# Optimization experiments

Measured on AMD Instinct MI355X. Metric: run time of the kernel, lower is better.

The kernel has to match this reference:

```python
import jax, jax.numpy as jnp
import numpy as np

H_DIM = 1024
MAX_T = 1024
N_HEADS = 16


def setup_inputs() -> dict:
    key = jax.random.key(0)
    ks = jax.random.split(key, 9)
    B, T, C = 4, 1024, H_DIM
    s = 1.0 / np.sqrt(C)
    return {
        "x": jax.random.normal(ks[0], (B, T, C), jnp.float32),
        "Wq": jax.random.normal(ks[1], (C, H_DIM), jnp.float32) * s,
        "bq": jnp.zeros((H_DIM,), jnp.float32),
        "Wk": jax.random.normal(ks[2], (C, H_DIM), jnp.float32) * s,
        "bk": jnp.zeros((H_DIM,), jnp.float32),
        "Wv": jax.random.normal(ks[3], (C, H_DIM), jnp.float32) * s,
        "bv": jnp.zeros((H_DIM,), jnp.float32),
        "Wo": jax.random.normal(ks[4], (H_DIM, H_DIM), jnp.float32) * s,
        "bo": jnp.zeros((H_DIM,), jnp.float32),
    }


def reference(x, Wq, bq, Wk, bk, Wv, bv, Wo, bo):
    B, T, C = x.shape
    N, D = N_HEADS, C // N_HEADS
    # QKV projections -> [B, N, T, D]
    def split_heads(y):
        return y.reshape(B, T, N, D).transpose(0, 2, 1, 3)
    q = split_heads(x @ Wq + bq)
    k = split_heads(x @ Wk + bk)
    v = split_heads(x @ Wv + bv)
    # scores [B, N, T, T]
    scores = jnp.einsum("bntd,bnsd->bnts", q, k) / jnp.sqrt(jnp.float32(D))
    # Faithful to source: -1e9 added on the LOWER-triangular positions
    mask = jnp.tril(jnp.ones((T, T), jnp.float32)) * (-1e9)
    scores = scores + mask[None, None, :, :]
    attn = jax.nn.softmax(scores, axis=-1)
    out = jnp.einsum("bnts,bnsd->bntd", attn, v)  # [B, N, T, D]
    out = out.transpose(0, 2, 1, 3).reshape(B, T, N * D)
    return out @ Wo + bo
```

## Files before the change

kernel.cpp:

```cpp
#include <hip/hip_runtime.h>
#include <hip/hip_bf16.h>
#include <stdint.h>

#define T_SEQ 1024
#define C_DIM 1024
#define NH 16
#define DH 64

typedef __attribute__((ext_vector_type(8))) __bf16 bf16x8;
typedef __attribute__((ext_vector_type(8))) uint16_t u16x8;
typedef __attribute__((ext_vector_type(4))) float f32x4;

__device__ __forceinline__ uint16_t f2bf(float f) {
    union { float f; uint32_t u; } v; v.f = f;
    uint32_t u = v.u;
    return (uint16_t)((u + 0x7FFFu + ((u >> 16) & 1u)) >> 16);
}
__device__ __forceinline__ float bf2f(uint16_t b) {
    union { uint32_t u; float f; } v; v.u = ((uint32_t)b) << 16; return v.f;
}

__global__ void k_prep(const float* __restrict__ x,
                       const float* __restrict__ W0, const float* __restrict__ W1,
                       const float* __restrict__ W2, const float* __restrict__ W3,
                       uint16_t* __restrict__ xb, uint16_t* __restrict__ wout) {
    const int gid = blockIdx.x;
    if (gid < 2048) {
        int i = gid * 256 + threadIdx.x;
        const int st = 2048 * 256;
#pragma unroll
        for (int it = 0; it < 2; it++, i += st) {
            float4 v = reinterpret_cast<const float4*>(x)[i];
            ushort4 o;
            o.x = f2bf(v.x); o.y = f2bf(v.y); o.z = f2bf(v.z); o.w = f2bf(v.w);
            reinterpret_cast<ushort4*>(xb)[i] = o;
        }
        return;
    }
    __shared__ float tile[32][33];
    const int id2 = gid - 2048;
    const int z = id2 >> 10;
    const int by = ((id2 >> 5) & 31) * 32;
    const int bx = (id2 & 31) * 32;
    const float* in = (z == 0) ? W0 : (z == 1) ? W1 : (z == 2) ? W2 : W3;
    uint16_t* o = wout + ((size_t)z << 20);
    const int tx = threadIdx.x & 31, ty = threadIdx.x >> 5;
#pragma unroll
    for (int i = 0; i < 4; i++)
        tile[ty + i * 8][tx] = in[(size_t)(by + ty + i * 8) * C_DIM + bx + tx];
    __syncthreads();
#pragma unroll
    for (int i = 0; i < 4; i++)
        o[(size_t)(bx + ty + i * 8) * C_DIM + by + tx] = f2bf(tile[tx][ty + i * 8]);
}

__global__ void k_vmean(const uint16_t* __restrict__ Vt, float* __restrict__ Vmean) {
    const int bh = blockIdx.x;
    const int tid = threadIdx.x;
    const int d = tid >> 2, part = tid & 3;
    const uint16_t* src = Vt + ((size_t)bh * DH + d) * T_SEQ + part * 256;
    float s = 0.f;
#pragma unroll
    for (int i = 0; i < 32; i++) {
        u16x8 v = *reinterpret_cast<const u16x8*>(src + i * 8);
#pragma unroll
        for (int j = 0; j < 8; j++) s += bf2f(v[j]);
    }
    s += __shfl_xor(s, 1);
    s += __shfl_xor(s, 2);
    if (part == 0) Vmean[bh * DH + d] = s * (1.0f / 1024.0f);
}

__device__ __forceinline__ void stage_g(const uint16_t* A, const uint16_t* Bt, int bm, int bn,
                                        int kt, char* la, char* lb, int tid) {
    const int w = tid >> 6, srow = tid >> 2;
    const int scol = (((tid & 3) ^ ((srow >> 1) & 3))) * 8;
#pragma unroll
    for (int p = 0; p < 2; p++) {
        const uint16_t* ga = A + (size_t)(bm + p * 64 + srow) * C_DIM + kt + scol;
        const uint16_t* gb = Bt + (size_t)(bn + p * 64 + srow) * C_DIM + kt + scol;
        __builtin_amdgcn_global_load_lds(
            (const __attribute__((address_space(1))) void*)ga,
            (__attribute__((address_space(3))) void*)(la + p * 4096 + w * 1024), 16, 0, 0);
        __builtin_amdgcn_global_load_lds(
            (const __attribute__((address_space(1))) void*)gb,
            (__attribute__((address_space(3))) void*)(lb + p * 4096 + w * 1024), 16, 0, 0);
    }
}

__global__ __launch_bounds__(256) void k_gemm_qkv(const uint16_t* __restrict__ A,
                                                  const uint16_t* __restrict__ Bt,
                                                  const float* __restrict__ bq,
                                                  const float* __restrict__ bk,
                                                  const float* __restrict__ bv,
                                                  uint16_t* __restrict__ qb,
                                                  uint16_t* __restrict__ kb,
                                                  uint16_t* __restrict__ vt) {
    __shared__ uint16_t lA[128 * 32];
    __shared__ uint16_t lB[128 * 32];
    const int bm = blockIdx.x * 128;
    const int bn = blockIdx.y * 128;
    const int tid = threadIdx.x;
    const int lane = tid & 63;
    const int w = tid >> 6;
    const int wm = (w >> 1) * 64;
    const int wn = (w & 1) * 64;
    const int ko = (lane >> 4) * 8;
    const int rr = lane & 15;
    const int pos = ko ^ (((rr >> 1) & 3) << 3);

    f32x4 acc[4][4] = {};

    for (int kt = 0; kt < C_DIM; kt += 32) {
        stage_g(A, Bt, bm, bn, kt, (char*)lA, (char*)lB, tid);
        __syncthreads();
        bf16x8 af[4], bfr[4];
#pragma unroll
        for (int i = 0; i < 4; i++) {
            af[i]  = *reinterpret_cast<const bf16x8*>(&lA[(wm + i * 16 + rr) * 32 + pos]);
            bfr[i] = *reinterpret_cast<const bf16x8*>(&lB[(wn + i * 16 + rr) * 32 + pos]);
        }
#pragma unroll
        for (int mi = 0; mi < 4; mi++)
#pragma unroll
            for (int ni = 0; ni < 4; ni++)
                acc[mi][ni] = __builtin_amdgcn_mfma_f32_16x16x32_bf16(af[mi], bfr[ni], acc[mi][ni], 0, 0, 0);
        __syncthreads();
    }

    const float* bias; uint16_t* outp; int coff, vmode;
    if (bn < 1024)      { bias = bq; outp = qb; coff = 0;    vmode = 0; }
    else if (bn < 2048) { bias = bk; outp = kb; coff = 1024; vmode = 0; }
    else                { bias = bv; outp = vt; coff = 2048; vmode = 1; }

    const int r0 = (lane >> 4) * 4;
    const int cc = lane & 15;
#pragma unroll
    for (int ni = 0; ni < 4; ni++) {
        const int colg = bn + wn + ni * 16 + cc;
        const int col = colg - coff;
        const float bvv = bias[col];
#pragma unroll
        for (int mi = 0; mi < 4; mi++) {
#pragma unroll
            for (int jj = 0; jj < 4; jj++) {
                const int row = bm + wm + mi * 16 + r0 + jj;
                float v = acc[mi][ni][jj] + bvv;
                if (vmode == 0) {
                    outp[(size_t)row * C_DIM + col] = f2bf(v);
                } else {
                    const int b = row >> 10, t2 = row & 1023;
                    const int h = col >> 6, d = col & 63;
                    outp[((size_t)((b * NH + h) * DH + d) << 10) + t2] = f2bf(v);
                }
            }
        }
    }
}

__global__ __launch_bounds__(256) void k_gemm_o(const uint16_t* __restrict__ A,
                                                const uint16_t* __restrict__ Bt,
                                                const float* __restrict__ bias,
                                                float* __restrict__ Out) {
    __shared__ uint16_t lA[128 * 32];
    __shared__ uint16_t lB[128 * 32];
    const int bm = blockIdx.x * 128;
    const int bn = blockIdx.y * 128;
    const int tid = threadIdx.x;
    const int lane = tid & 63;
    const int w = tid >> 6;
    const int wm = (w >> 1) * 64;
    const int wn = (w & 1) * 64;
    const int ko = (lane >> 4) * 8;
    const int rr = lane & 15;
    const int pos = ko ^ (((rr >> 1) & 3) << 3);

    f32x4 acc[4][4] = {};

    for (int kt = 0; kt < C_DIM; kt += 32) {
        stage_g(A, Bt, bm, bn, kt, (char*)lA, (char*)lB, tid);
        __syncthreads();
        bf16x8 af[4], bfr[4];
#pragma unroll
        for (int i = 0; i < 4; i++) {
            af[i]  = *reinterpret_cast<const bf16x8*>(&lA[(wm + i * 16 + rr) * 32 + pos]);
            bfr[i] = *reinterpret_cast<const bf16x8*>(&lB[(wn + i * 16 + rr) * 32 + pos]);
        }
#pragma unroll
        for (int mi = 0; mi < 4; mi++)
#pragma unroll
            for (int ni = 0; ni < 4; ni++)
                acc[mi][ni] = __builtin_amdgcn_mfma_f32_16x16x32_bf16(af[mi], bfr[ni], acc[mi][ni], 0, 0, 0);
        __syncthreads();
    }

    const int r0 = (lane >> 4) * 4;
    const int cc = lane & 15;
#pragma unroll
    for (int ni = 0; ni < 4; ni++) {
        const int col = bn + wn + ni * 16 + cc;
        const float bvv = bias[col];
#pragma unroll
        for (int mi = 0; mi < 4; mi++)
#pragma unroll
            for (int jj = 0; jj < 4; jj++) {
                const int row = bm + wm + mi * 16 + r0 + jj;
                Out[(size_t)row * C_DIM + col] = acc[mi][ni][jj] + bvv;
            }
    }
}

__global__ __launch_bounds__(256, 3) void k_attn(const uint16_t* __restrict__ Q,
                                                 const uint16_t* __restrict__ Kb,
                                                 const uint16_t* __restrict__ Vt,
                                                 const float* __restrict__ Vmean,
                                                 uint16_t* __restrict__ Ob) {
    __shared__ char smem[32768 + 4 * 4608];
    const int tid = threadIdx.x;
    const int lane = tid & 63;
    const int w = tid >> 6;
    uint16_t* lpLo = reinterpret_cast<uint16_t*>(smem + 32768 + w * 4608);
    uint16_t* lpHi = lpLo + 1152;

    const int id = blockIdx.x;
    const int bh = id & 63;
    const int braw = id >> 6;
    const int b = (braw < 4) ? braw : 11 - braw;
    const int q0 = b * 128;
    const int bb = bh >> 4, h = bh & 15;
    const int qq = lane & 15;
    const int gg = lane >> 4;
    const int ko = gg * 8;
    const int r0 = gg * 4;
    const int qgLo = q0 + w * 32 + qq;
    const int qgHi = qgLo + 16;

    const uint16_t* qpLo = Q + (size_t)(bb * T_SEQ + qgLo) * C_DIM + h * DH + ko;
    const uint16_t* qpHi = Q + (size_t)(bb * T_SEQ + qgHi) * C_DIM + h * DH + ko;
    bf16x8 bqLo0 = *reinterpret_cast<const bf16x8*>(qpLo);
    bf16x8 bqLo1 = *reinterpret_cast<const bf16x8*>(qpLo + 32);
    bf16x8 bqHi0 = *reinterpret_cast<const bf16x8*>(qpHi);
    bf16x8 bqHi1 = *reinterpret_cast<const bf16x8*>(qpHi + 32);

    const uint16_t* kbase = Kb + (size_t)bb * T_SEQ * C_DIM + h * DH;
    const uint16_t* vbase = Vt + (size_t)bh * DH * T_SEQ;
    const uint16_t* KL = reinterpret_cast<const uint16_t*>(smem);
    const uint16_t* VL = reinterpret_cast<const uint16_t*>(smem + 16384);

    f32x4 oLo[4] = {}, oHi[4] = {};
    float llLo = 0.f, llHi = 0.f;
    const float zs = 0.125f * 1.44269504088896f;

    const int sz = (qq & 7) << 3;

    const int t0 = b;
    for (int t = t0; t < 8; t++) {
        const int s0 = t * 128;
#pragma unroll
        for (int i = 0; i < 4; i++) {
            const int r = i * 32 + (tid >> 3);
            const int sc = ((tid & 7) ^ (r & 7)) * 8;
            const uint16_t* ks = kbase + (size_t)(s0 + r) * C_DIM + sc;
            __builtin_amdgcn_global_load_lds(
                (const __attribute__((address_space(1))) void*)ks,
                (__attribute__((address_space(3))) void*)(smem + i * 4096 + w * 1024), 16, 0, 0);
        }
#pragma unroll
        for (int i = 0; i < 4; i++) {
            const int r = i * 16 + (tid >> 4);
            const int sc = ((tid & 15) ^ (r & 7)) * 8;
            const uint16_t* vs = vbase + (size_t)r * T_SEQ + s0 + sc;
            __builtin_amdgcn_global_load_lds(
                (const __attribute__((address_space(1))) void*)vs,
                (__attribute__((address_space(3))) void*)(smem + 16384 + i * 4096 + w * 1024), 16, 0, 0);
        }
        __syncthreads();

        uint32_t* lpLo32 = reinterpret_cast<uint32_t*>(lpLo);
        uint32_t* lpHi32 = reinterpret_cast<uint32_t*>(lpHi);
#pragma unroll
        for (int h2 = 0; h2 < 2; h2++) {
#pragma unroll
            for (int hf = 0; hf < 4; hf++) {
                const int rr = h2 * 64 + hf * 16 + qq;
                bf16x8 kf0 = *reinterpret_cast<const bf16x8*>(&KL[rr * 64 + (ko ^ sz)]);
                bf16x8 kf1 = *reinterpret_cast<const bf16x8*>(&KL[rr * 64 + ((32 + ko) ^ sz)]);
                f32x4 sLo = {}, sHi = {};
                sLo = __builtin_amdgcn_mfma_f32_16x16x32_bf16(kf0, bqLo0, sLo, 0, 0, 0);
                sLo = __builtin_amdgcn_mfma_f32_16x16x32_bf16(kf1, bqLo1, sLo, 0, 0, 0);
                sHi = __builtin_amdgcn_mfma_f32_16x16x32_bf16(kf0, bqHi0, sHi, 0, 0, 0);
                sHi = __builtin_amdgcn_mfma_f32_16x16x32_bf16(kf1, bqHi1, sHi, 0, 0, 0);
#pragma unroll
                for (int j = 0; j < 4; j++) {
                    const int k = s0 + h2 * 64 + hf * 16 + r0 + j;
                    const float zLo = sLo[j] * zs + ((k <= qgLo) ? -1e9f : 0.0f);
                    const float zHi = sHi[j] * zs + ((k <= qgHi) ? -1e9f : 0.0f);
                    const float pLo = __builtin_amdgcn_exp2f(zLo);
                    const float pHi = __builtin_amdgcn_exp2f(zHi);
                    sLo[j] = pLo; llLo += pLo;
                    sHi[j] = pHi; llHi += pHi;
                }
#pragma unroll
                for (int jp = 0; jp < 2; jp++) {
                    union { __hip_bfloat162 h2u; uint32_t u; } cL, cH;
                    cL.h2u = __float22bfloat162_rn(make_float2(sLo[2 * jp], sLo[2 * jp + 1]));
                    cH.h2u = __float22bfloat162_rn(make_float2(sHi[2 * jp], sHi[2 * jp + 1]));
                    lpLo32[qq * 36 + hf * 8 + (r0 >> 1) + jp] = cL.u;
                    lpHi32[qq * 36 + hf * 8 + (r0 >> 1) + jp] = cH.u;
                }
            }
            bf16x8 paLo0 = *reinterpret_cast<const bf16x8*>(&lpLo[qq * 72 + ko]);
            bf16x8 paLo1 = *reinterpret_cast<const bf16x8*>(&lpLo[qq * 72 + 32 + ko]);
            bf16x8 paHi0 = *reinterpret_cast<const bf16x8*>(&lpHi[qq * 72 + ko]);
            bf16x8 paHi1 = *reinterpret_cast<const bf16x8*>(&lpHi[qq * 72 + 32 + ko]);
#pragma unroll
            for (int ni = 0; ni < 4; ni++) {
                const int rr = ni * 16 + qq;
                bf16x8 vf0 = *reinterpret_cast<const bf16x8*>(&VL[rr * 128 + ((h2 * 64 + ko) ^ sz)]);
                bf16x8 vf1 = *reinterpret_cast<const bf16x8*>(&VL[rr * 128 + ((h2 * 64 + 32 + ko) ^ sz)]);
                oLo[ni] = __builtin_amdgcn_mfma_f32_16x16x32_bf16(paLo0, vf0, oLo[ni], 0, 0, 0);
                oLo[ni] = __builtin_amdgcn_mfma_f32_16x16x32_bf16(paLo1, vf1, oLo[ni], 0, 0, 0);
                oHi[ni] = __builtin_amdgcn_mfma_f32_16x16x32_bf16(paHi0, vf0, oHi[ni], 0, 0, 0);
                oHi[ni] = __builtin_amdgcn_mfma_f32_16x16x32_bf16(paHi1, vf1, oHi[ni], 0, 0, 0);
            }
        }
        __syncthreads();
    }

    llLo += __shfl_xor(llLo, 16); llLo += __shfl_xor(llLo, 32);
    llHi += __shfl_xor(llHi, 16); llHi += __shfl_xor(llHi, 32);
#pragma unroll
    for (int j = 0; j < 4; j++) {
        {
            const float lr = __shfl(llLo, r0 + j);
            const size_t row = (size_t)(bb * T_SEQ + q0 + w * 32 + r0 + j);
            if (lr > 0.f) {
                const float rinv = 1.0f / lr;
#pragma unroll
                for (int ni = 0; ni < 4; ni++)
                    Ob[row * C_DIM + h * DH + ni * 16 + qq] = f2bf(oLo[ni][j] * rinv);
            } else {
#pragma unroll
                for (int ni = 0; ni < 4; ni++)
                    Ob[row * C_DIM + h * DH + ni * 16 + qq] = f2bf(Vmean[bh * DH + ni * 16 + qq]);
            }
        }
        {
            const float lr = __shfl(llHi, r0 + j);
            const size_t row = (size_t)(bb * T_SEQ + q0 + w * 32 + 16 + r0 + j);
            if (lr > 0.f) {
                const float rinv = 1.0f / lr;
#pragma unroll
                for (int ni = 0; ni < 4; ni++)
                    Ob[row * C_DIM + h * DH + ni * 16 + qq] = f2bf(oHi[ni][j] * rinv);
            } else {
#pragma unroll
                for (int ni = 0; ni < 4; ni++)
                    Ob[row * C_DIM + h * DH + ni * 16 + qq] = f2bf(Vmean[bh * DH + ni * 16 + qq]);
            }
        }
    }
}

extern "C" void kernel_launch(void* const* d_in, const int* in_sizes, int n_in,
                              void* d_out, int out_size, void* d_ws, size_t ws_size,
                              hipStream_t stream) {
    const float* x  = (const float*)d_in[0];
    const float* Wq = (const float*)d_in[1];
    const float* bq = (const float*)d_in[2];
    const float* Wk = (const float*)d_in[3];
    const float* bk = (const float*)d_in[4];
    const float* Wv = (const float*)d_in[5];
    const float* bv = (const float*)d_in[6];
    const float* Wo = (const float*)d_in[7];
    const float* bo = (const float*)d_in[8];
    float* out = (float*)d_out;

    char* ws = (char*)d_ws;
    uint16_t* xb    = (uint16_t*)(ws);
    uint16_t* wqkvt = (uint16_t*)(ws + (8u  << 20));
    float*    vmean = (float*)   (ws + (12u << 20));
    uint16_t* qb    = (uint16_t*)(ws + (16u << 20));
    uint16_t* kb    = (uint16_t*)(ws + (24u << 20));
    uint16_t* vt    = (uint16_t*)(ws + (32u << 20));
    uint16_t* wot   = wqkvt + (3u << 20);
    uint16_t* ab    = qb;

    k_prep<<<6144, 256, 0, stream>>>(x, Wq, Wk, Wv, Wo, xb, wqkvt);

    k_gemm_qkv<<<dim3(32, 24), 256, 0, stream>>>(xb, wqkvt, bq, bk, bv, qb, kb, vt);
    k_vmean<<<64, 256, 0, stream>>>(vt, vmean);
    k_attn<<<512, 256, 0, stream>>>(qb, kb, vt, vmean, ab);
    k_gemm_o<<<dim3(32, 8), 256, 0, stream>>>(ab, wot, bo, out);
}
```

Baseline: 103.2 us.

## Double-buffer LDS in QKV and output GEMMs to overlap global loads with MFMA

Replaces the single-buffered K-loop in both projection GEMMs with a two-stage LDS ping-pong. The next K-tile is fetched via global_load_lds while MFMAs run on the current tile, and waiting is done with an explicit vmcnt(4) plus raw s_barrier. This aims to hide global-load latency that previously stalled every iteration. It doubles LDS use per block, which may lower occupancy, and the hand-counted vmcnt depends on stage_g issuing exactly four loads.

```diff
diff --git a/kernel.cpp b/kernel.cpp
--- a/kernel.cpp
+++ b/kernel.cpp
@@ -88,6 +88,37 @@
     }
 }
 
+#define GEMM_KLOOP(LA, LB)                                                        \
+    stage_g(A, Bt, bm, bn, 0, (char*)LA[0], (char*)LB[0], tid);                   \
+    for (int kt = 0; kt < 32; kt++) {                                             \
+        const int c = kt & 1;                                                     \
+        if (kt < 31) {                                                            \
+            stage_g(A, Bt, bm, bn, (kt + 1) * 32, (char*)LA[c ^ 1], (char*)LB[c ^ 1], tid); \
+            __builtin_amdgcn_sched_barrier(0);                                    \
+            asm volatile("s_waitcnt vmcnt(4)" ::: "memory");                      \
+        } else {                                                                  \
+            __builtin_amdgcn_sched_barrier(0);                                    \
+            asm volatile("s_waitcnt vmcnt(0)" ::: "memory");                      \
+        }                                                                         \
+        __builtin_amdgcn_sched_barrier(0);                                        \
+        __builtin_amdgcn_s_barrier();       \
+        __builtin_amdgcn_sched_barrier(0);                                        \
+        bf16x8 af[4], bfr[4];                                                     \
+        _Pragma("unroll")                                                         \
+        for (int i = 0; i < 4; i++) {                                             \
+            af[i]  = *reinterpret_cast<const bf16x8*>(&LA[c][(wm + i * 16 + rr) * 32 + pos]); \
+            bfr[i] = *reinterpret_cast<const bf16x8*>(&LB[c][(wn + i * 16 + rr) * 32 + pos]); \
+        }                                                                         \
+        _Pragma("unroll")                                                         \
+        for (int mi = 0; mi < 4; mi++)                                            \
+            _Pragma("unroll")                                                     \
+            for (int ni = 0; ni < 4; ni++)                                        \
+                acc[mi][ni] = __builtin_amdgcn_mfma_f32_16x16x32_bf16(af[mi], bfr[ni], acc[mi][ni], 0, 0, 0); \
+        __builtin_amdgcn_sched_barrier(0);                                        \
+        __builtin_amdgcn_s_barrier();       \
+        __builtin_amdgcn_sched_barrier(0);                                        \
+    }
+
 __global__ __launch_bounds__(256) void k_gemm_qkv(const uint16_t* __restrict__ A,
                                                   const uint16_t* __restrict__ Bt,
                                                   const float* __restrict__ bq,
@@ -96,8 +127,8 @@
                                                   uint16_t* __restrict__ qb,
                                                   uint16_t* __restrict__ kb,
                                                   uint16_t* __restrict__ vt) {
-    __shared__ uint16_t lA[128 * 32];
-    __shared__ uint16_t lB[128 * 32];
+    __shared__ uint16_t lA[2][128 * 32];
+    __shared__ uint16_t lB[2][128 * 32];
     const int bm = blockIdx.x * 128;
     const int bn = blockIdx.y * 128;
     const int tid = threadIdx.x;
@@ -111,22 +142,7 @@
 
     f32x4 acc[4][4] = {};
 
-    for (int kt = 0; kt < C_DIM; kt += 32) {
-        stage_g(A, Bt, bm, bn, kt, (char*)lA, (char*)lB, tid);
-        __syncthreads();
-        bf16x8 af[4], bfr[4];
-#pragma unroll
-        for (int i = 0; i < 4; i++) {
-            af[i]  = *reinterpret_cast<const bf16x8*>(&lA[(wm + i * 16 + rr) * 32 + pos]);
-            bfr[i] = *reinterpret_cast<const bf16x8*>(&lB[(wn + i * 16 + rr) * 32 + pos]);
-        }
-#pragma unroll
-        for (int mi = 0; mi < 4; mi++)
-#pragma unroll
-            for (int ni = 0; ni < 4; ni++)
-                acc[mi][ni] = __builtin_amdgcn_mfma_f32_16x16x32_bf16(af[mi], bfr[ni], acc[mi][ni], 0, 0, 0);
-        __syncthreads();
-    }
+    GEMM_KLOOP(lA, lB)
 
     const float* bias; uint16_t* outp; int coff, vmode;
     if (bn < 1024)      { bias = bq; outp = qb; coff = 0;    vmode = 0; }
@@ -162,8 +178,8 @@
                                                 const uint16_t* __restrict__ Bt,
                                                 const float* __restrict__ bias,
                                                 float* __restrict__ Out) {
-    __shared__ uint16_t lA[128 * 32];
-    __shared__ uint16_t lB[128 * 32];
+    __shared__ uint16_t lA[2][128 * 32];
+    __shared__ uint16_t lB[2][128 * 32];
     const int bm = blockIdx.x * 128;
     const int bn = blockIdx.y * 128;
     const int tid = threadIdx.x;
@@ -177,22 +193,7 @@
 
     f32x4 acc[4][4] = {};
 
-    for (int kt = 0; kt < C_DIM; kt += 32) {
-        stage_g(A, Bt, bm, bn, kt, (char*)lA, (char*)lB, tid);
-        __syncthreads();
-        bf16x8 af[4], bfr[4];
-#pragma unroll
-        for (int i = 0; i < 4; i++) {
-            af[i]  = *reinterpret_cast<const bf16x8*>(&lA[(wm + i * 16 + rr) * 32 + pos]);
-            bfr[i] = *reinterpret_cast<const bf16x8*>(&lB[(wn + i * 16 + rr) * 32 + pos]);
-        }
-#pragma unroll
-        for (int mi = 0; mi < 4; mi++)
-#pragma unroll
-            for (int ni = 0; ni < 4; ni++)
-                acc[mi][ni] = __builtin_amdgcn_mfma_f32_16x16x32_bf16(af[mi], bfr[ni], acc[mi][ni], 0, 0, 0);
-        __syncthreads();
-    }
+    GEMM_KLOOP(lA, lB)
 
     const int r0 = (lane >> 4) * 4;
     const int cc = lane & 15;
```

New measurement: 106.8 us. 3.6% more time.

## Rewrite QKV GEMM with 256x256 tiles and double-buffered async LDS pipeline

Applied to the files above, without the earlier changes.

Replaces the 128x128, K=32 single-buffered QKV GEMM with a 512-thread kernel computing 256x256 tiles with K=64 steps, double-buffered LDS filled by global_load_lds and staged in quarters interleaved with MFMA phases. It uses explicit vmcnt waits, XOR swizzling, and setprio around MFMA bursts to overlap loads with compute and improve operand reuse. The trade-off is only 192 blocks on the device and large LDS use, which reduces occupancy and may leave compute units idle.

```diff
diff --git a/kernel.cpp b/kernel.cpp
--- a/kernel.cpp
+++ b/kernel.cpp
@@ -69,6 +69,133 @@
     s += __shfl_xor(s, 1);
     s += __shfl_xor(s, 2);
     if (part == 0) Vmean[bh * DH + d] = s * (1.0f / 1024.0f);
+}
+
+__device__ __forceinline__ void stage_half(const uint16_t* __restrict__ src, int rowbase,
+                                           int kt, char* ldsbase, int tid) {
+    const int wid = tid >> 6;
+#pragma unroll
+    for (int i = 0; i < 2; i++) {
+        const int r = i * 64 + (tid >> 3);
+        const int sch = (tid & 7) ^ (r & 7);
+        const uint16_t* g = src + (size_t)(rowbase + r) * C_DIM + kt * 64 + sch * 8;
+        __builtin_amdgcn_global_load_lds(
+            (const __attribute__((address_space(1))) void*)g,
+            (__attribute__((address_space(3))) void*)(ldsbase + i * 8192 + wid * 1024),
+            16, 0, 0);
+    }
+}
+
+__global__ __launch_bounds__(512) void k_gemm_qkv(const uint16_t* __restrict__ A,
+                                                  const uint16_t* __restrict__ Bt,
+                                                  const float* __restrict__ bq,
+                                                  const float* __restrict__ bk,
+                                                  const float* __restrict__ bv,
+                                                  uint16_t* __restrict__ qb,
+                                                  uint16_t* __restrict__ kb,
+                                                  uint16_t* __restrict__ vt) {
+    __shared__ uint16_t lA[2][256 * 64];
+    __shared__ uint16_t lB[2][256 * 64];
+    const int tid = threadIdx.x;
+    const int lane = tid & 63;
+    const int wid = tid >> 6;
+    const int wr = wid >> 2;
+    const int wc = wid & 3;
+    const int bm = blockIdx.x * 256;
+    const int bn = blockIdx.y * 256;
+    const int qq = lane & 15;
+    const int gg = lane >> 4;
+    const int r0 = gg * 4;
+
+    f32x4 acc[8][4] = {};
+
+    stage_half(A,  bm,       0, (char*)lA[0],         tid);
+    stage_half(A,  bm + 128, 0, (char*)lA[0] + 16384, tid);
+    stage_half(Bt, bn,       0, (char*)lB[0],         tid);
+    stage_half(Bt, bn + 128, 0, (char*)lB[0] + 16384, tid);
+
+#pragma unroll 1
+    for (int kt = 0; kt < 16; kt++) {
+        const int c = kt & 1;
+        const uint16_t* LAc = lA[c];
+        const uint16_t* LBc = lB[c];
+        char* LAn = (char*)lA[c ^ 1];
+        char* LBn = (char*)lB[c ^ 1];
+#pragma unroll
+        for (int p = 0; p < 4; p++) {
+            if (kt < 15) {
+                if (p == 0) stage_half(A,  bm,       kt + 1, LAn,         tid);
+                if (p == 1) stage_half(A,  bm + 128, kt + 1, LAn + 16384, tid);
+                if (p == 2) stage_half(Bt, bn,       kt + 1, LBn,         tid);
+                if (p == 3) stage_half(Bt, bn + 128, kt + 1, LBn + 16384, tid);
+            }
+            if (p == 0) {
+                __builtin_amdgcn_sched_barrier(0);
+                if (kt < 15) asm volatile("s_waitcnt vmcnt(2)" ::: "memory");
+                else         asm volatile("s_waitcnt vmcnt(0)" ::: "memory");
+                __builtin_amdgcn_sched_barrier(0);
+            }
+            __builtin_amdgcn_s_barrier();
+            const int mh = p >> 1, nh = p & 1;
+            bf16x8 af[4][2], bfr[2][2];
+#pragma unroll
+            for (int m = 0; m < 4; m++) {
+                const int row = wr * 128 + mh * 64 + m * 16 + qq;
+#pragma unroll
+                for (int kk = 0; kk < 2; kk++) {
+                    const int pos = ((kk * 4 + gg) ^ (qq & 7)) * 8;
+                    af[m][kk] = *reinterpret_cast<const bf16x8*>(&LAc[row * 64 + pos]);
+                }
+            }
+#pragma unroll
+            for (int n = 0; n < 2; n++) {
+                const int row = wc * 64 + nh * 32 + n * 16 + qq;
+#pragma unroll
+                for (int kk = 0; kk < 2; kk++) {
+                    const int pos = ((kk * 4 + gg) ^ (qq & 7)) * 8;
+                    bfr[n][kk] = *reinterpret_cast<const bf16x8*>(&LBc[row * 64 + pos]);
+                }
+            }
+            __builtin_amdgcn_s_setprio(1);
+#pragma unroll
+            for (int m = 0; m < 4; m++)
+#pragma unroll
+                for (int n = 0; n < 2; n++)
+#pragma unroll
+                    for (int kk = 0; kk < 2; kk++)
+                        acc[mh * 4 + m][nh * 2 + n] = __builtin_amdgcn_mfma_f32_16x16x32_bf16(
+                            af[m][kk], bfr[n][kk], acc[mh * 4 + m][nh * 2 + n], 0, 0, 0);
+            __builtin_amdgcn_s_setprio(0);
+            __builtin_amdgcn_s_barrier();
+        }
+    }
+
+    const float* bias; uint16_t* outp; int coff, vmode;
+    if (bn < 1024)      { bias = bq; outp = qb; coff = 0;    vmode = 0; }
+    else if (bn < 2048) { bias = bk; outp = kb; coff = 1024; vmode = 0; }
+    else                { bias = bv; outp = vt; coff = 2048; vmode = 1; }
+
+#pragma unroll
+    for (int n = 0; n < 4; n++) {
+        const int colg = bn + wc * 64 + n * 16 + qq;
+        const int col = colg - coff;
+        const float bvv = bias[col];
+#pragma unroll
+        for (int mi = 0; mi < 8; mi++) {
+#pragma unroll
+            for (int jj = 0; jj < 4; jj++) {
+                const int row = bm + wr * 128 + (mi >> 2) * 64 + (mi & 3) * 16 + r0 + jj;
+                float v = acc[mi][n][jj] + bvv;
+                if (vmode == 0) {
+                    outp[(size_t)row * C_DIM + col] = f2bf(v);
+                } else {
+                    const int b = row >> 10, t2 = row & 1023;
+                    const int h = col >> 6, d = col & 63;
+                    outp[((size_t)((b * NH + h) * DH + d) << 10) + t2] = f2bf(v);
+                }
+            }
+        }
+    }
 }
 
 __device__ __forceinline__ void stage_g(const uint16_t* A, const uint16_t* Bt, int bm, int bn,
@@ -85,76 +212,6 @@
         __builtin_amdgcn_global_load_lds(
             (const __attribute__((address_space(1))) void*)gb,
             (__attribute__((address_space(3))) void*)(lb + p * 4096 + w * 1024), 16, 0, 0);
-    }
-}
-
-__global__ __launch_bounds__(256) void k_gemm_qkv(const uint16_t* __restrict__ A,
-                                                  const uint16_t* __restrict__ Bt,
-                                                  const float* __restrict__ bq,
-                                                  const float* __restrict__ bk,
-                                                  const float* __restrict__ bv,
-                                                  uint16_t* __restrict__ qb,
-                                                  uint16_t* __restrict__ kb,
-                                                  uint16_t* __restrict__ vt) {
-    __shared__ uint16_t lA[128 * 32];
-    __shared__ uint16_t lB[128 * 32];
-    const int bm = blockIdx.x * 128;
-    const int bn = blockIdx.y * 128;
-    const int tid = threadIdx.x;
-    const int lane = tid & 63;
-    const int w = tid >> 6;
-    const int wm = (w >> 1) * 64;
-    const int wn = (w & 1) * 64;
-    const int ko = (lane >> 4) * 8;
-    const int rr = lane & 15;
-    const int pos = ko ^ (((rr >> 1) & 3) << 3);
-
-    f32x4 acc[4][4] = {};
-
-    for (int kt = 0; kt < C_DIM; kt += 32) {
-        stage_g(A, Bt, bm, bn, kt, (char*)lA, (char*)lB, tid);
-        __syncthreads();
-        bf16x8 af[4], bfr[4];
-#pragma unroll
-        for (int i = 0; i < 4; i++) {
-            af[i]  = *reinterpret_cast<const bf16x8*>(&lA[(wm + i * 16 + rr) * 32 + pos]);
-            bfr[i] = *reinterpret_cast<const bf16x8*>(&lB[(wn + i * 16 + rr) * 32 + pos]);
-        }
-#pragma unroll
-        for (int mi = 0; mi < 4; mi++)
-#pragma unroll
-            for (int ni = 0; ni < 4; ni++)
-                acc[mi][ni] = __builtin_amdgcn_mfma_f32_16x16x32_bf16(af[mi], bfr[ni], acc[mi][ni], 0, 0, 0);
-        __syncthreads();
-    }
-
-    const float* bias; uint16_t* outp; int coff, vmode;
-    if (bn < 1024)      { bias = bq; outp = qb; coff = 0;    vmode = 0; }
-    else if (bn < 2048) { bias = bk; outp = kb; coff = 1024; vmode = 0; }
-    else                { bias = bv; outp = vt; coff = 2048; vmode = 1; }
-
-    const int r0 = (lane >> 4) * 4;
-    const int cc = lane & 15;
-#pragma unroll
-    for (int ni = 0; ni < 4; ni++) {
-        const int colg = bn + wn + ni * 16 + cc;
-        const int col = colg - coff;
-        const float bvv = bias[col];
-#pragma unroll
-        for (int mi = 0; mi < 4; mi++) {
-#pragma unroll
-            for (int jj = 0; jj < 4; jj++) {
-                const int row = bm + wm + mi * 16 + r0 + jj;
-                float v = acc[mi][ni][jj] + bvv;
-                if (vmode == 0) {
-                    outp[(size_t)row * C_DIM + col] = f2bf(v);
-                } else {
-                    const int b = row >> 10, t2 = row & 1023;
-                    const int h = col >> 6, d = col & 63;
-                    outp[((size_t)((b * NH + h) * DH + d) << 10) + t2] = f2bf(v);
-                }
-            }
-        }
     }
 }
 
@@ -388,7 +445,7 @@
 
     k_prep<<<6144, 256, 0, stream>>>(x, Wq, Wk, Wv, Wo, xb, wqkvt);
 
-    k_gemm_qkv<<<dim3(32, 24), 256, 0, stream>>>(xb, wqkvt, bq, bk, bv, qb, kb, vt);
+    k_gemm_qkv<<<dim3(16, 12), 512, 0, stream>>>(xb, wqkvt, bq, bk, bv, qb, kb, vt);
     k_vmean<<<64, 256, 0, stream>>>(vt, vmean);
     k_attn<<<512, 256, 0, stream>>>(qb, kb, vt, vmean, ab);
     k_gemm_o<<<dim3(32, 8), 256, 0, stream>>>(ab, wot, bo, out);
```

New measurement: 142.7 us. 1.38x slower.

## Double-buffer K tiles in LDS and load V fragments directly from global

Applied to the files above, without the earlier changes.

The attention kernel now prefetches the next K tile into a second LDS buffer while computing on the current one, and drops the trailing barrier. V fragments are read straight from global memory into registers instead of being staged in LDS. On the first (diagonal) tile, waves whose queries fall entirely in the masked region skip the first half. This overlaps K loading with compute and cuts LDS traffic, at the cost of uncoalesced-ish global V reads and more register pressure.

```diff
diff --git a/kernel.cpp b/kernel.cpp
--- a/kernel.cpp
+++ b/kernel.cpp
@@ -244,8 +244,6 @@
 
     const uint16_t* kbase = Kb + (size_t)bb * T_SEQ * C_DIM + h * DH;
     const uint16_t* vbase = Vt + (size_t)bh * DH * T_SEQ;
-    const uint16_t* KL = reinterpret_cast<const uint16_t*>(smem);
-    const uint16_t* VL = reinterpret_cast<const uint16_t*>(smem + 16384);
 
     f32x4 oLo[4] = {}, oHi[4] = {};
     float llLo = 0.f, llHi = 0.f;
@@ -254,32 +252,46 @@
     const int sz = (qq & 7) << 3;
 
     const int t0 = b;
+#pragma unroll
+    for (int i = 0; i < 4; i++) {
+        const int r = i * 32 + (tid >> 3);
+        const int sc = ((tid & 7) ^ (r & 7)) * 8;
+        const uint16_t* ks = kbase + (size_t)(t0 * 128 + r) * C_DIM + sc;
+        __builtin_amdgcn_global_load_lds(
+            (const __attribute__((address_space(1))) void*)ks,
+            (__attribute__((address_space(3))) void*)(smem + i * 4096 + w * 1024), 16, 0, 0);
+    }
+
     for (int t = t0; t < 8; t++) {
+        const int cur = (t - t0) & 1;
+        __syncthreads();
+        if (t + 1 < 8) {
+            char* nb = smem + (cur ^ 1) * 16384;
+#pragma unroll
+            for (int i = 0; i < 4; i++) {
+                const int r = i * 32 + (tid >> 3);
+                const int sc = ((tid & 7) ^ (r & 7)) * 8;
+                const uint16_t* ks = kbase + (size_t)((t + 1) * 128 + r) * C_DIM + sc;
+                __builtin_amdgcn_global_load_lds(
+                    (const __attribute__((address_space(1))) void*)ks,
+                    (__attribute__((address_space(3))) void*)(nb + i * 4096 + w * 1024), 16, 0, 0);
+            }
+        }
         const int s0 = t * 128;
-#pragma unroll
-        for (int i = 0; i < 4; i++) {
-            const int r = i * 32 + (tid >> 3);
-            const int sc = ((tid & 7) ^ (r & 7)) * 8;
-            const uint16_t* ks = kbase + (size_t)(s0 + r) * C_DIM + sc;
-            __builtin_amdgcn_global_load_lds(
-                (const __attribute__((address_space(1))) void*)ks,
-                (__attribute__((address_space(3))) void*)(smem + i * 4096 + w * 1024), 16, 0, 0);
-        }
-#pragma unroll
-        for (int i = 0; i < 4; i++) {
-            const int r = i * 16 + (tid >> 4);
-            const int sc = ((tid & 15) ^ (r & 7)) * 8;
-            const uint16_t* vs = vbase + (size_t)r * T_SEQ + s0 + sc;
-            __builtin_amdgcn_global_load_lds(
-                (const __attribute__((address_space(1))) void*)vs,
-                (__attribute__((address_space(3))) void*)(smem + 16384 + i * 4096 + w * 1024), 16, 0, 0);
-        }
-        __syncthreads();
+        const uint16_t* KL = reinterpret_cast<const uint16_t*>(smem + cur * 16384);
 
         uint32_t* lpLo32 = reinterpret_cast<uint32_t*>(lpLo);
         uint32_t* lpHi32 = reinterpret_cast<uint32_t*>(lpHi);
 #pragma unroll
         for (int h2 = 0; h2 < 2; h2++) {
+            if (t == t0 && h2 == 0 && w >= 2) continue;
+            bf16x8 vf[4][2];
+#pragma unroll
+            for (int ni = 0; ni < 4; ni++) {
+                const uint16_t* vp = vbase + (size_t)(ni * 16 + qq) * T_SEQ + s0 + h2 * 64 + ko;
+                vf[ni][0] = *reinterpret_cast<const bf16x8*>(vp);
+                vf[ni][1] = *reinterpret_cast<const bf16x8*>(vp + 32);
+            }
 #pragma unroll
             for (int hf = 0; hf < 4; hf++) {
                 const int rr = h2 * 64 + hf * 16 + qq;
@@ -315,16 +327,12 @@
             bf16x8 paHi1 = *reinterpret_cast<const bf16x8*>(&lpHi[qq * 72 + 32 + ko]);
 #pragma unroll
             for (int ni = 0; ni < 4; ni++) {
-                const int rr = ni * 16 + qq;
-                bf16x8 vf0 = *reinterpret_cast<const bf16x8*>(&VL[rr * 128 + ((h2 * 64 + ko) ^ sz)]);
-                bf16x8 vf1 = *reinterpret_cast<const bf16x8*>(&VL[rr * 128 + ((h2 * 64 + 32 + ko) ^ sz)]);
-                oLo[ni] = __builtin_amdgcn_mfma_f32_16x16x32_bf16(paLo0, vf0, oLo[ni], 0, 0, 0);
-                oLo[ni] = __builtin_amdgcn_mfma_f32_16x16x32_bf16(paLo1, vf1, oLo[ni], 0, 0, 0);
-                oHi[ni] = __builtin_amdgcn_mfma_f32_16x16x32_bf16(paHi0, vf0, oHi[ni], 0, 0, 0);
-                oHi[ni] = __builtin_amdgcn_mfma_f32_16x16x32_bf16(paHi1, vf1, oHi[ni], 0, 0, 0);
-            }
-        }
-        __syncthreads();
+                oLo[ni] = __builtin_amdgcn_mfma_f32_16x16x32_bf16(paLo0, vf[ni][0], oLo[ni], 0, 0, 0);
+                oLo[ni] = __builtin_amdgcn_mfma_f32_16x16x32_bf16(paLo1, vf[ni][1], oLo[ni], 0, 0, 0);
+                oHi[ni] = __builtin_amdgcn_mfma_f32_16x16x32_bf16(paHi0, vf[ni][0], oHi[ni], 0, 0, 0);
+                oHi[ni] = __builtin_amdgcn_mfma_f32_16x16x32_bf16(paHi1, vf[ni][1], oHi[ni], 0, 0, 0);
+            }
+        }
     }
 
     llLo += __shfl_xor(llLo, 16); llLo += __shfl_xor(llLo, 32);
```

Result: slower. 107.8 us (+4.5%).
